# Kernel tuning notes

Hardware: AMD Instinct MI355X
Metric: run time of the kernel (lower is better)

## Reference

```python
import jax, jax.numpy as jnp
import numpy as np

N = 100000   # nodes
E = 1600000  # edges per view
B = 256      # graphs in batch
D = 128      # feature dim
H, C = 4, 32 # heads, per-head channels (H*C = 128)


def _seg_softmax(logits, seg, num_seg):
    # numerically stable softmax over segments (per-destination / per-graph)
    m = jax.ops.segment_max(logits, seg, num_segments=num_seg)
    e = jnp.exp(logits - m[seg])
    s = jax.ops.segment_sum(e, seg, num_segments=num_seg)
    return e / s[seg]


def _gat_conv(x, edge_index, W, att_src, att_dst, bias):
    # PyG GATConv with add_self_loops=True, concat heads
    n = x.shape[0]
    loop = jnp.arange(n, dtype=edge_index.dtype)
    src = jnp.concatenate([edge_index[0], loop])
    dst = jnp.concatenate([edge_index[1], loop])
    xh = (x @ W).reshape(n, H, C)                      # [N,H,C]
    a_src = jnp.einsum('nhc,hc->nh', xh, att_src)      # [N,H]
    a_dst = jnp.einsum('nhc,hc->nh', xh, att_dst)
    alpha = jax.nn.leaky_relu(a_src[src] + a_dst[dst], 0.2)   # [E+N,H]
    alpha = _seg_softmax(alpha, dst, n)
    msg = xh[src] * alpha[..., None]                   # [E+N,H,C]
    out = jax.ops.segment_sum(msg, dst, num_segments=n)
    return out.reshape(n, H * C) + bias


def _global_attention(h, batch, gate_W, gate_b):
    gate = (h @ gate_W + gate_b)[:, 0]                 # [N]
    a = _seg_softmax(gate, batch, B)
    return jax.ops.segment_sum(a[:, None] * h, batch, num_segments=B)  # [B,128]


def setup_inputs() -> dict:
    key = jax.random.key(0)
    ks = jax.random.split(key, 32)
    p = lambda k, shp: (jax.random.normal(k, shp, dtype=jnp.float32) * 0.05)
    inp = {
        'x': jax.random.normal(ks[0], (N, D), dtype=jnp.float32),
        'edge_index_ast': jax.random.randint(ks[1], (2, E), 0, N, dtype=jnp.int32),
        'edge_index_cfg': jax.random.randint(ks[2], (2, E), 0, N, dtype=jnp.int32),
        'edge_index_pdg': jax.random.randint(ks[3], (2, E), 0, N, dtype=jnp.int32),
        'batch': jnp.sort(jax.random.randint(ks[4], (N,), 0, B, dtype=jnp.int32)),
        'ln_g': jnp.ones((D,), jnp.float32),
        'ln_b': jnp.zeros((D,), jnp.float32),
        'proj_W': p(ks[5], (D, D)), 'proj_b': p(ks[6], (D,)),
        'W_ast': p(ks[7], (D, H * C)), 'att_src_ast': p(ks[8], (H, C)), 'att_dst_ast': p(ks[9], (H, C)), 'bias_ast': p(ks[10], (H * C,)),
        'W_cfg': p(ks[11], (D, H * C)), 'att_src_cfg': p(ks[12], (H, C)), 'att_dst_cfg': p(ks[13], (H, C)), 'bias_cfg': p(ks[14], (H * C,)),
        'W_pdg': p(ks[15], (D, H * C)), 'att_src_pdg': p(ks[16], (H, C)), 'att_dst_pdg': p(ks[17], (H, C)), 'bias_pdg': p(ks[18], (H * C,)),
        'gate_W': p(ks[19], (H * C, 1)), 'gate_b': p(ks[20], (1,)),
        'clf_W1': p(ks[21], (3 * H * C, 128)), 'clf_b1': p(ks[22], (128,)),
        'clf_W2': p(ks[23], (128, 1)), 'clf_b2': p(ks[24], (1,)),
    }
    return inp


def reference(x, edge_index_ast, edge_index_cfg, edge_index_pdg, batch,
              ln_g, ln_b, proj_W, proj_b,
              W_ast, att_src_ast, att_dst_ast, bias_ast,
              W_cfg, att_src_cfg, att_dst_cfg, bias_cfg,
              W_pdg, att_src_pdg, att_dst_pdg, bias_pdg,
              gate_W, gate_b, clf_W1, clf_b1, clf_W2, clf_b2):
    # LayerNorm + proj + LeakyReLU (dropout = eval/no-op)
    mu = jnp.mean(x, axis=-1, keepdims=True)
    var = jnp.var(x, axis=-1, keepdims=True)
    xn = (x - mu) * jax.lax.rsqrt(var + 1e-5) * ln_g + ln_b
    h0 = jax.nn.leaky_relu(xn @ proj_W + proj_b, 0.01)

    h_ast = jax.nn.elu(_gat_conv(h0, edge_index_ast, W_ast, att_src_ast, att_dst_ast, bias_ast))
    g_ast = _global_attention(h_ast, batch, gate_W, gate_b)
    h_cfg = jax.nn.elu(_gat_conv(h0, edge_index_cfg, W_cfg, att_src_cfg, att_dst_cfg, bias_cfg))
    g_cfg = _global_attention(h_cfg, batch, gate_W, gate_b)
    h_pdg = jax.nn.elu(_gat_conv(h0, edge_index_pdg, W_pdg, att_src_pdg, att_dst_pdg, bias_pdg))
    g_pdg = _global_attention(h_pdg, batch, gate_W, gate_b)

    combined = jnp.concatenate([g_ast, g_cfg, g_pdg], axis=1)  # [B, 384]
    hid = jax.nn.leaky_relu(combined @ clf_W1 + clf_b1, 0.01)
    return (hid @ clf_W2 + clf_b2).reshape(-1)                 # [B]
```

## Files before the change

kernel.cpp:

```cpp
#include <hip/hip_runtime.h>
#include <hip/hip_bf16.h>
#include <hip/hip_fp16.h>
#include <math.h>

#define NN 100000
#define EE 1600000
#define BB 256
#define NBUCK 391
#define PBLK 384
#define CH 4167
#define TOTB (3 * PBLK)
#define ROWS_PAD 100096
#define SCAP 4608
#define OBCAP (SCAP + 256)
#define LOG2E 1.442695041f
#define GEMM_BLKS 782
#define AGG_BLKS 25000
#define XH_ELEMS ((size_t)ROWS_PAD * 128)
#define A_ELEMS ((size_t)ROWS_PAD * 4)
#define HV_ELEMS ((size_t)NN * 128)

typedef short bf16x8 __attribute__((ext_vector_type(8)));
typedef float f32x4 __attribute__((ext_vector_type(4)));

__device__ __forceinline__ unsigned short f2bf(float f) {
    __hip_bfloat16 h = __float2bfloat16(f);
    return *(unsigned short*)&h;
}
__device__ __forceinline__ unsigned short f2h(float f) {
    __half h = __float2half(f);
    return *(unsigned short*)&h;
}
__device__ __forceinline__ float h2f(unsigned short u) {
    __half h = *(__half*)&u;
    return __half2float(h);
}

__global__ __launch_bounds__(256) void prep_kernel(const float* __restrict__ W0,
                                                   const float* __restrict__ W1,
                                                   const float* __restrict__ W2,
                                                   const float* __restrict__ W3,
                                                   const float* __restrict__ ln_g,
                                                   const float* __restrict__ ln_b,
                                                   unsigned short* __restrict__ WT,
                                                   float* __restrict__ c12) {
    if (blockIdx.x < 256) {
        int which = blockIdx.x >> 6;
        const float* W = which == 0 ? W0 : which == 1 ? W1 : which == 2 ? W2 : W3;
        int i = (blockIdx.x & 63) * 256 + threadIdx.x;
        int n = i >> 7, k = i & 127;
        float v = W[k * 128 + n];
        if (which == 0) v *= ln_g[k];
        WT[which * 16384 + i] = f2bf(v);
        return;
    }
    __shared__ float p1[256], p2[256];
    int t = threadIdx.x;
    int n = t & 127, kg = t >> 7;
    float c1 = 0.f, c2 = 0.f;
    for (int k = kg * 64; k < kg * 64 + 64; k++) {
        float w = W0[k * 128 + n];
        c1 = fmaf(ln_g[k], w, c1);
        c2 = fmaf(ln_b[k], w, c2);
    }
    p1[t] = c1; p2[t] = c2;
    __syncthreads();
    if (kg == 0) {
        c12[n] = p1[n] + p1[128 + n];
        c12[128 + n] = p2[n] + p2[128 + n];
    }
}


__device__ __forceinline__ void scatter_res_body(int bid, int tid,
                                                 const int* __restrict__ e0,
                                                 const int* __restrict__ e1,
                                                 const int* __restrict__ e2,
                                                 int* __restrict__ counters,
                                                 unsigned int* __restrict__ pairbuf) {
    int v = bid / PBLK, p = bid % PBLK;
    const int* ei = v == 0 ? e0 : v == 1 ? e1 : e2;
    __shared__ int hcnt[NBUCK];
    __shared__ int cur[NBUCK];
    for (int i = tid; i < NBUCK; i += 256) hcnt[i] = 0;
    __syncthreads();
    int ea = p * CH, ebnd = min(EE, ea + CH);
    int e = ea + tid;
    for (; e + 768 < ebnd; e += 1024) {
        int d0 = ei[EE + e], d1 = ei[EE + e + 256];
        int d2 = ei[EE + e + 512], d3 = ei[EE + e + 768];
        atomicAdd(&hcnt[((unsigned)d0) >> 8], 1);
        atomicAdd(&hcnt[((unsigned)d1) >> 8], 1);
        atomicAdd(&hcnt[((unsigned)d2) >> 8], 1);
        atomicAdd(&hcnt[((unsigned)d3) >> 8], 1);
    }
    for (; e < ebnd; e += 256) atomicAdd(&hcnt[((unsigned)ei[EE + e]) >> 8], 1);
    __syncthreads();
    int* gcnt = counters + v * NBUCK;
    for (int i = tid; i < NBUCK; i += 256) {
        int c = hcnt[i];
        cur[i] = c ? atomicAdd(&gcnt[i], c) : 0;
    }
    __syncthreads();
    unsigned int* pbuf = pairbuf + (size_t)v * NBUCK * SCAP;
    e = ea + tid;
    for (; e + 768 < ebnd; e += 1024) {
        unsigned s0 = (unsigned)ei[e],       d0 = (unsigned)ei[EE + e];
        unsigned s1 = (unsigned)ei[e + 256], d1 = (unsigned)ei[EE + e + 256];
        unsigned s2 = (unsigned)ei[e + 512], d2 = (unsigned)ei[EE + e + 512];
        unsigned s3 = (unsigned)ei[e + 768], d3 = (unsigned)ei[EE + e + 768];
        int p0 = atomicAdd(&cur[d0 >> 8], 1);
        int p1 = atomicAdd(&cur[d1 >> 8], 1);
        int p2 = atomicAdd(&cur[d2 >> 8], 1);
        int p3 = atomicAdd(&cur[d3 >> 8], 1);
        if (p0 < SCAP) pbuf[(size_t)(d0 >> 8) * SCAP + p0] = (s0 << 8) | (d0 & 255u);
        if (p1 < SCAP) pbuf[(size_t)(d1 >> 8) * SCAP + p1] = (s1 << 8) | (d1 & 255u);
        if (p2 < SCAP) pbuf[(size_t)(d2 >> 8) * SCAP + p2] = (s2 << 8) | (d2 & 255u);
        if (p3 < SCAP) pbuf[(size_t)(d3 >> 8) * SCAP + p3] = (s3 << 8) | (d3 & 255u);
    }
    for (; e < ebnd; e += 256) {
        unsigned s = (unsigned)ei[e], d = (unsigned)ei[EE + e];
        int pos = atomicAdd(&cur[d >> 8], 1);
        if (pos < SCAP) pbuf[(size_t)(d >> 8) * SCAP + pos] = (s << 8) | (d & 255u);
    }
}

__device__ __forceinline__ void proj_body(int nb, int tid,
                                          const float* __restrict__ X,
                                          const unsigned short* __restrict__ WT,
                                          const float* __restrict__ c12,
                                          const float* __restrict__ pb,
                                          unsigned short* __restrict__ Out) {
    int w = tid >> 6, lane = tid & 63;
    int ln = lane & 15, oct = lane >> 4;
    int row0 = nb * 128 + w * 32;

    f32x4 acc[2][8];
    #pragma unroll
    for (int i = 0; i < 2; i++)
        #pragma unroll
        for (int j = 0; j < 8; j++) acc[i][j] = (f32x4){0.f, 0.f, 0.f, 0.f};

    const float* X0 = X + (size_t)min(row0 + ln, NN - 1) * 128;
    const float* X1 = X + (size_t)min(row0 + 16 + ln, NN - 1) * 128;
    const bf16x8* Wr = (const bf16x8*)(WT + (size_t)ln * 128);

    float s0 = 0.f, q0 = 0.f, s1 = 0.f, q1 = 0.f;
    #pragma unroll
    for (int kq = 0; kq < 4; kq++) {
        int koff = kq * 4 + oct;
        float4 xa = *(const float4*)(X0 + koff * 8);
        float4 xb = *(const float4*)(X0 + koff * 8 + 4);
        float4 ya = *(const float4*)(X1 + koff * 8);
        float4 yb = *(const float4*)(X1 + koff * 8 + 4);
        s0 += (xa.x + xa.y) + (xa.z + xa.w) + (xb.x + xb.y) + (xb.z + xb.w);
        q0 += xa.x * xa.x + xa.y * xa.y + xa.z * xa.z + xa.w * xa.w
            + xb.x * xb.x + xb.y * xb.y + xb.z * xb.z + xb.w * xb.w;
        s1 += (ya.x + ya.y) + (ya.z + ya.w) + (yb.x + yb.y) + (yb.z + yb.w);
        q1 += ya.x * ya.x + ya.y * ya.y + ya.z * ya.z + ya.w * ya.w
            + yb.x * yb.x + yb.y * yb.y + yb.z * yb.z + yb.w * yb.w;
        bf16x8 a0, a1;
        a0[0] = (short)f2bf(xa.x); a0[1] = (short)f2bf(xa.y); a0[2] = (short)f2bf(xa.z); a0[3] = (short)f2bf(xa.w);
        a0[4] = (short)f2bf(xb.x); a0[5] = (short)f2bf(xb.y); a0[6] = (short)f2bf(xb.z); a0[7] = (short)f2bf(xb.w);
        a1[0] = (short)f2bf(ya.x); a1[1] = (short)f2bf(ya.y); a1[2] = (short)f2bf(ya.z); a1[3] = (short)f2bf(ya.w);
        a1[4] = (short)f2bf(yb.x); a1[5] = (short)f2bf(yb.y); a1[6] = (short)f2bf(yb.z); a1[7] = (short)f2bf(yb.w);
        #pragma unroll
        for (int ct = 0; ct < 8; ct++) {
            bf16x8 bfr = Wr[ct * 16 * 16 + koff];
            acc[0][ct] = __builtin_amdgcn_mfma_f32_16x16x32_bf16(a0, bfr, acc[0][ct], 0, 0, 0);
            acc[1][ct] = __builtin_amdgcn_mfma_f32_16x16x32_bf16(a1, bfr, acc[1][ct], 0, 0, 0);
        }
    }
    #pragma unroll
    for (int m = 16; m < 64; m <<= 1) {
        s0 += __shfl_xor(s0, m); q0 += __shfl_xor(q0, m);
        s1 += __shfl_xor(s1, m); q1 += __shfl_xor(q1, m);
    }
    float mu0 = s0 * (1.0f / 128.0f);
    float rs0 = rsqrtf(q0 * (1.0f / 128.0f) - mu0 * mu0 + 1e-5f);
    float mu1 = s1 * (1.0f / 128.0f);
    float rs1 = rsqrtf(q1 * (1.0f / 128.0f) - mu1 * mu1 + 1e-5f);

    float c1v[8], c2v[8], pbv[8];
    #pragma unroll
    for (int ct = 0; ct < 8; ct++) {
        c1v[ct] = c12[ct * 16 + ln];
        c2v[ct] = c12[128 + ct * 16 + ln];
        pbv[ct] = pb[ct * 16 + ln];
    }
    #pragma unroll
    for (int rt = 0; rt < 2; rt++) {
        #pragma unroll
        for (int r = 0; r < 4; r++) {
            int src = oct * 4 + r;
            float rs_r = __shfl(rt ? rs1 : rs0, src);
            float mu_r = __shfl(rt ? mu1 : mu0, src);
            int row = row0 + rt * 16 + oct * 4 + r;
            #pragma unroll
            for (int ct = 0; ct < 8; ct++) {
                float v = rs_r * acc[rt][ct][r] - rs_r * mu_r * c1v[ct] + c2v[ct] + pbv[ct];
                v = v > 0.f ? v : 0.01f * v;
                Out[(size_t)row * 128 + ct * 16 + ln] = f2bf(v);
            }
        }
    }
}

__device__ __forceinline__ void view_body(int nb, int tid,
                                          const unsigned short* __restrict__ h0,
                                          const unsigned short* __restrict__ WTv,
                                          const float* __restrict__ asw,
                                          const float* __restrict__ adw,
                                          unsigned short* __restrict__ Out,
                                          float* __restrict__ a_src,
                                          float* __restrict__ a_dst) {
    int w = tid >> 6, lane = tid & 63;
    int ln = lane & 15, oct = lane >> 4;
    int row0 = nb * 128 + w * 32;

    f32x4 acc[2][8];
    #pragma unroll
    for (int i = 0; i < 2; i++)
        #pragma unroll
        for (int j = 0; j < 8; j++) acc[i][j] = (f32x4){0.f, 0.f, 0.f, 0.f};

    const bf16x8* Ar0 = (const bf16x8*)(h0 + (size_t)(row0 + ln) * 128);
    const bf16x8* Ar1 = (const bf16x8*)(h0 + (size_t)(row0 + 16 + ln) * 128);
    const bf16x8* Wr  = (const bf16x8*)(WTv + (size_t)ln * 128);

    #pragma unroll
    for (int kq = 0; kq < 4; kq++) {
        int koff = kq * 4 + oct;
        bf16x8 a0 = Ar0[koff];
        bf16x8 a1 = Ar1[koff];
        #pragma unroll
        for (int ct = 0; ct < 8; ct++) {
            bf16x8 bfr = Wr[ct * 16 * 16 + koff];
            acc[0][ct] = __builtin_amdgcn_mfma_f32_16x16x32_bf16(a0, bfr, acc[0][ct], 0, 0, 0);
            acc[1][ct] = __builtin_amdgcn_mfma_f32_16x16x32_bf16(a1, bfr, acc[1][ct], 0, 0, 0);
        }
    }
    float aswv[8], adwv[8];
    #pragma unroll
    for (int ct = 0; ct < 8; ct++) {
        aswv[ct] = asw[ct * 16 + ln] * LOG2E;
        adwv[ct] = adw[ct * 16 + ln] * LOG2E;
    }

    #pragma unroll
    for (int rt = 0; rt < 2; rt++) {
        #pragma unroll
        for (int r = 0; r < 4; r++) {
            int row = row0 + rt * 16 + oct * 4 + r;
            float sh_[4] = {0.f, 0.f, 0.f, 0.f}, dh_[4] = {0.f, 0.f, 0.f, 0.f};
            #pragma unroll
            for (int ct = 0; ct < 8; ct++) {
                float vv = acc[rt][ct][r];
                Out[(size_t)row * 128 + ct * 16 + ln] = f2h(vv);
                sh_[ct >> 1] = fmaf(vv, aswv[ct], sh_[ct >> 1]);
                dh_[ct >> 1] = fmaf(vv, adwv[ct], dh_[ct >> 1]);
            }
            #pragma unroll
            for (int off = 1; off < 16; off <<= 1) {
                #pragma unroll
                for (int h = 0; h < 4; h++) {
                    sh_[h] += __shfl_xor(sh_[h], off);
                    dh_[h] += __shfl_xor(dh_[h], off);
                }
            }
            if (ln == 0) {
                *(float4*)(a_src + (size_t)row * 4) = make_float4(sh_[0], sh_[1], sh_[2], sh_[3]);
                *(float4*)(a_dst + (size_t)row * 4) = make_float4(dh_[0], dh_[1], dh_[2], dh_[3]);
            }
        }
    }
}

__device__ __forceinline__ void fine_body(int bid, int t,
                                          const unsigned int* __restrict__ pairbuf,
                                          const int* __restrict__ counters,
                                          int* __restrict__ deg3,
                                          int* __restrict__ start3,
                                          unsigned int* __restrict__ ebuf3) {
    int v = bid / NBUCK, b = bid - v * NBUCK;
    int cnt = min(counters[v * NBUCK + b], SCAP);
    const unsigned int* pb = pairbuf + (size_t)(v * NBUCK + b) * SCAP;
    unsigned int* eb = ebuf3 + (size_t)(v * NBUCK + b) * OBCAP;
    int obase = (v * NBUCK + b) * OBCAP;
    __shared__ int hist[256], cur[256];
    __shared__ int wsum[4];
    int node = b * 256 + t;
    int valid = (node < NN) ? 1 : 0;
    hist[t] = valid;
    __syncthreads();
    {
        int i = t;
        for (; i + 768 < cnt; i += 1024) {
            unsigned v0 = pb[i], v1 = pb[i + 256], v2 = pb[i + 512], v3 = pb[i + 768];
            atomicAdd(&hist[v0 & 255u], 1);
            atomicAdd(&hist[v1 & 255u], 1);
            atomicAdd(&hist[v2 & 255u], 1);
            atomicAdd(&hist[v3 & 255u], 1);
        }
        for (; i < cnt; i += 256) atomicAdd(&hist[pb[i] & 255u], 1);
    }
    __syncthreads();
    int hv = hist[t];
    int lanev = t & 63, wv = t >> 6;
    int incl = hv;
    #pragma unroll
    for (int m = 1; m < 64; m <<= 1) {
        int u = __shfl_up(incl, m);
        if (lanev >= m) incl += u;
    }
    if (lanev == 63) wsum[wv] = incl;
    __syncthreads();
    int prefix = 0;
    #pragma unroll
    for (int i = 0; i < 4; i++) prefix += (i < wv) ? wsum[i] : 0;
    int excl = incl + prefix - hv;
    cur[t] = excl + valid;
    if (valid) eb[excl] = (((unsigned)node) << 8) | ((unsigned)node & 255u);
    __syncthreads();
    {
        int i = t;
        for (; i + 768 < cnt; i += 1024) {
            unsigned v0 = pb[i], v1 = pb[i + 256], v2 = pb[i + 512], v3 = pb[i + 768];
            int p0 = atomicAdd(&cur[v0 & 255u], 1);
            int p1 = atomicAdd(&cur[v1 & 255u], 1);
            int p2 = atomicAdd(&cur[v2 & 255u], 1);
            int p3 = atomicAdd(&cur[v3 & 255u], 1);
            eb[p0] = v0; eb[p1] = v1; eb[p2] = v2; eb[p3] = v3;
        }
        for (; i < cnt; i += 256) {
            unsigned int val = pb[i];
            int pos = atomicAdd(&cur[val & 255u], 1);
            eb[pos] = val;
        }
    }
    if (valid) {
        deg3[v * NN + node] = hv;
        start3[v * NN + node] = obase + excl;
    }
}

__device__ __forceinline__ void agg_body(int node, int tid,
                                         const unsigned short* __restrict__ xh,
                                         const int* __restrict__ start,
                                         const int* __restrict__ deg,
                                         const unsigned int* __restrict__ ebuf,
                                         const float* __restrict__ a_src,
                                         const float* __restrict__ a_dst,
                                         const float* __restrict__ bias,
                                         const float* __restrict__ gw,
                                         const float* __restrict__ gb,
                                         unsigned short* __restrict__ hvb,
                                         float* __restrict__ gexpv,
                                         float* wlds) {
    int lane = tid & 63;
    int h = lane >> 4;
    int st = start[node];
    int cnt = deg[node];
    const char* xb = (const char*)xh;
    int laneoff = lane * 4;
    float4 ad4 = *(const float4*)(a_dst + (size_t)node * 4);
    float* ww = wlds + (tid >> 6) * 272;
    const float* wr = ww + h * 68;

    float accx = 0.f, accy = 0.f, den = 0.f;
    for (int j0 = 0; j0 < cnt; j0 += 64) {
        int nj = min(64, cnt - j0);
        int src_l = 0;
        if (lane < nj) {
            src_l = (int)(ebuf[st + j0 + lane] >> 8);
            float4 as4 = *(const float4*)(a_src + (size_t)src_l * 4);
            float t0 = as4.x + ad4.x, t1 = as4.y + ad4.y;
            float t2 = as4.z + ad4.z, t3 = as4.w + ad4.w;
            t0 = fmaxf(t0, 0.f) + 0.2f * fminf(t0, 0.f);
            t1 = fmaxf(t1, 0.f) + 0.2f * fminf(t1, 0.f);
            t2 = fmaxf(t2, 0.f) + 0.2f * fminf(t2, 0.f);
            t3 = fmaxf(t3, 0.f) + 0.2f * fminf(t3, 0.f);
            ww[0 * 68 + lane] = exp2f(t0);
            ww[1 * 68 + lane] = exp2f(t1);
            ww[2 * 68 + lane] = exp2f(t2);
            ww[3 * 68 + lane] = exp2f(t3);
        }
        int jj = 0;
        for (; jj + 8 <= nj; jj += 8) {
            int s0 = __builtin_amdgcn_readlane(src_l, jj);
            int s1 = __builtin_amdgcn_readlane(src_l, jj + 1);
            int s2 = __builtin_amdgcn_readlane(src_l, jj + 2);
            int s3 = __builtin_amdgcn_readlane(src_l, jj + 3);
            int s4 = __builtin_amdgcn_readlane(src_l, jj + 4);
            int s5 = __builtin_amdgcn_readlane(src_l, jj + 5);
            int s6 = __builtin_amdgcn_readlane(src_l, jj + 6);
            int s7 = __builtin_amdgcn_readlane(src_l, jj + 7);
            __half2 x0 = *(const __half2*)(xb + (((size_t)(unsigned)s0) << 8) + laneoff);
            __half2 x1 = *(const __half2*)(xb + (((size_t)(unsigned)s1) << 8) + laneoff);
            __half2 x2 = *(const __half2*)(xb + (((size_t)(unsigned)s2) << 8) + laneoff);
            __half2 x3 = *(const __half2*)(xb + (((size_t)(unsigned)s3) << 8) + laneoff);
            __half2 x4 = *(const __half2*)(xb + (((size_t)(unsigned)s4) << 8) + laneoff);
            __half2 x5 = *(const __half2*)(xb + (((size_t)(unsigned)s5) << 8) + laneoff);
            __half2 x6 = *(const __half2*)(xb + (((size_t)(unsigned)s6) << 8) + laneoff);
            __half2 x7 = *(const __half2*)(xb + (((size_t)(unsigned)s7) << 8) + laneoff);
            float4 wa = *(const float4*)(wr + jj);
            float4 wb = *(const float4*)(wr + jj + 4);
            den += (wa.x + wa.y) + (wa.z + wa.w) + (wb.x + wb.y) + (wb.z + wb.w);
            accx = fmaf(__low2float(x0), wa.x, accx);
            accy = fmaf(__high2float(x0), wa.x, accy);
            accx = fmaf(__low2float(x1), wa.y, accx);
            accy = fmaf(__high2float(x1), wa.y, accy);
            accx = fmaf(__low2float(x2), wa.z, accx);
            accy = fmaf(__high2float(x2), wa.z, accy);
            accx = fmaf(__low2float(x3), wa.w, accx);
            accy = fmaf(__high2float(x3), wa.w, accy);
            accx = fmaf(__low2float(x4), wb.x, accx);
            accy = fmaf(__high2float(x4), wb.x, accy);
            accx = fmaf(__low2float(x5), wb.y, accx);
            accy = fmaf(__high2float(x5), wb.y, accy);
            accx = fmaf(__low2float(x6), wb.z, accx);
            accy = fmaf(__high2float(x6), wb.z, accy);
            accx = fmaf(__low2float(x7), wb.w, accx);
            accy = fmaf(__high2float(x7), wb.w, accy);
        }
        for (; jj + 4 <= nj; jj += 4) {
            int s0 = __builtin_amdgcn_readlane(src_l, jj);
            int s1 = __builtin_amdgcn_readlane(src_l, jj + 1);
            int s2 = __builtin_amdgcn_readlane(src_l, jj + 2);
            int s3 = __builtin_amdgcn_readlane(src_l, jj + 3);
            __half2 x0 = *(const __half2*)(xb + (((size_t)(unsigned)s0) << 8) + laneoff);
            __half2 x1 = *(const __half2*)(xb + (((size_t)(unsigned)s1) << 8) + laneoff);
            __half2 x2 = *(const __half2*)(xb + (((size_t)(unsigned)s2) << 8) + laneoff);
            __half2 x3 = *(const __half2*)(xb + (((size_t)(unsigned)s3) << 8) + laneoff);
            float4 wa = *(const float4*)(wr + jj);
            den += (wa.x + wa.y) + (wa.z + wa.w);
            accx = fmaf(__low2float(x0), wa.x, accx);
            accy = fmaf(__high2float(x0), wa.x, accy);
            accx = fmaf(__low2float(x1), wa.y, accx);
            accy = fmaf(__high2float(x1), wa.y, accy);
            accx = fmaf(__low2float(x2), wa.z, accx);
            accy = fmaf(__high2float(x2), wa.z, accy);
            accx = fmaf(__low2float(x3), wa.w, accx);
            accy = fmaf(__high2float(x3), wa.w, accy);
        }
        for (; jj < nj; jj++) {
            int s = __builtin_amdgcn_readlane(src_l, jj);
            float w = wr[jj];
            __half2 xv = *(const __half2*)(xb + (((size_t)(unsigned)s) << 8) + laneoff);
            den += w;
            accx = fmaf(__low2float(xv), w, accx);
            accy = fmaf(__high2float(xv), w, accy);
        }
    }
    float inv = 1.0f / den;
    float2 bb = *(const float2*)(bias + lane * 2);
    float o0 = accx * inv + bb.x;
    float o1 = accy * inv + bb.y;
    o0 = o0 > 0.f ? o0 : exp2f(o0 * LOG2E) - 1.0f;
    o1 = o1 > 0.f ? o1 : exp2f(o1 * LOG2E) - 1.0f;
    unsigned int packed = (unsigned)f2h(o0) | ((unsigned)f2h(o1) << 16);
    *(unsigned int*)(hvb + (size_t)node * 128 + lane * 2) = packed;
    float2 g2 = *(const float2*)(gw + lane * 2);
    float gp = o0 * g2.x + o1 * g2.y;
    #pragma unroll
    for (int m = 1; m < 64; m <<= 1) gp += __shfl_xor(gp, m);
    if (lane == 0) gexpv[node] = exp2f((gp + gb[0]) * LOG2E);
}

__device__ __forceinline__ void pool_body(int b, int tid,
                                          const unsigned short* __restrict__ hvb,
                                          const float* __restrict__ gexpv,
                                          const int* __restrict__ batch,
                                          float* __restrict__ gout,
                                          int voff,
                                          float* sacc, float* sws) {
    int g = tid >> 7;
    int ch = tid & 127;
    int l = 0, r = NN;
    while (l < r) { int m = (l + r) >> 1; if (batch[m] < b) l = m + 1; else r = m; }
    int s0 = l;
    r = NN;
    while (l < r) { int m = (l + r) >> 1; if (batch[m] < b + 1) l = m + 1; else r = m; }
    int s1 = l;
    float acc = 0.f, wsum = 0.f;
    for (int n = s0 + g; n < s1; n += 8) {
        float w = gexpv[n];
        wsum += w;
        acc = fmaf(w, h2f(hvb[(size_t)n * 128 + ch]), acc);
    }
    sacc[g * 128 + ch] = acc;
    if (ch == 0) sws[g] = wsum;
    __syncthreads();
    if (g == 0) {
        float a = 0.f, w = 0.f;
        #pragma unroll
        for (int i = 0; i < 8; i++) { a += sacc[i * 128 + ch]; w += sws[i]; }
        gout[b * 384 + voff + ch] = (s1 > s0) ? a / w : 0.f;
    }
}

__global__ __launch_bounds__(256) void fat_scatter_proj(const int* e0, const int* e1, const int* e2,
                                                        int* counters, unsigned int* pairbuf,
                                                        const float* X, const unsigned short* WT,
                                                        const float* c12, const float* pb,
                                                        unsigned short* h0) {
    if (blockIdx.x < TOTB) scatter_res_body(blockIdx.x, threadIdx.x, e0, e1, e2, counters, pairbuf);
    else proj_body(blockIdx.x - TOTB, threadIdx.x, X, WT, c12, pb, h0);
}

__global__ __launch_bounds__(256) void fat_fine_view3(const unsigned int* pairbuf, const int* counters,
                                                      int* deg3, int* start3, unsigned int* ebuf3,
                                                      const unsigned short* h0, const unsigned short* WT,
                                                      const float* as0, const float* ad0,
                                                      const float* as1, const float* ad1,
                                                      const float* as2, const float* ad2,
                                                      unsigned short* xh3, float* a_src3, float* a_dst3) {
    if (blockIdx.x < 3 * NBUCK) {
        fine_body(blockIdx.x, threadIdx.x, pairbuf, counters, deg3, start3, ebuf3);
        return;
    }
    int t = blockIdx.x - 3 * NBUCK;
    int v = t / GEMM_BLKS;
    int nb = t - v * GEMM_BLKS;
    const float* as_ = v == 0 ? as0 : v == 1 ? as1 : as2;
    const float* ad_ = v == 0 ? ad0 : v == 1 ? ad1 : ad2;
    view_body(nb, threadIdx.x, h0, WT + (size_t)(1 + v) * 16384, as_, ad_,
              xh3 + (size_t)v * XH_ELEMS,
              a_src3 + (size_t)v * A_ELEMS, a_dst3 + (size_t)v * A_ELEMS);
}

__global__ __launch_bounds__(256) void aggregate3_kernel(const unsigned short* __restrict__ xh3,
                                                         const int* __restrict__ start3,
                                                         const int* __restrict__ deg3,
                                                         const unsigned int* __restrict__ ebuf3,
                                                         const float* __restrict__ a_src3,
                                                         const float* __restrict__ a_dst3,
                                                         const float* __restrict__ b0,
                                                         const float* __restrict__ b1,
                                                         const float* __restrict__ b2,
                                                         const float* __restrict__ gw,
                                                         const float* __restrict__ gb,
                                                         unsigned short* __restrict__ hvb3,
                                                         float* __restrict__ gexpv3) {
    __shared__ float wlds[4 * 272];
    int v = blockIdx.x / AGG_BLKS;
    int bin = blockIdx.x - v * AGG_BLKS;
    int node = (bin * 256 + threadIdx.x) >> 6;
    if (node >= NN) return;
    const float* bias = v == 0 ? b0 : v == 1 ? b1 : b2;
    agg_body(node, threadIdx.x,
             xh3 + (size_t)v * XH_ELEMS,
             start3 + v * NN, deg3 + v * NN,
             ebuf3,
             a_src3 + (size_t)v * A_ELEMS, a_dst3 + (size_t)v * A_ELEMS,
             bias, gw, gb,
             hvb3 + (size_t)v * HV_ELEMS, gexpv3 + v * NN, wlds);
}

__global__ __launch_bounds__(1024) void pool3_kernel(const unsigned short* __restrict__ hvb3,
                                                     const float* __restrict__ gexpv3,
                                                     const int* __restrict__ batch,
                                                     float* __restrict__ gout) {
    __shared__ float sacc[8 * 128];
    __shared__ float sws[8];
    int v = blockIdx.x >> 8;
    int b = blockIdx.x & 255;
    pool_body(b, threadIdx.x, hvb3 + (size_t)v * HV_ELEMS, gexpv3 + v * NN,
              batch, gout, v * 128, sacc, sws);
}

__global__ __launch_bounds__(128) void clf_kernel(const float* __restrict__ gout,
                                                  const float* __restrict__ W1,
                                                  const float* __restrict__ b1,
                                                  const float* __restrict__ W2,
                                                  const float* __restrict__ b2,
                                                  float* __restrict__ out) {
    int b = blockIdx.x;
    int j = threadIdx.x;
    float acc = b1[j];
    for (int k = 0; k < 384; k++) acc = fmaf(gout[b * 384 + k], W1[k * 128 + j], acc);
    acc = acc > 0.f ? acc : 0.01f * acc;
    float p = acc * W2[j];
    #pragma unroll
    for (int m = 1; m < 64; m <<= 1) p += __shfl_xor(p, m);
    __shared__ float sh[2];
    if ((j & 63) == 0) sh[j >> 6] = p;
    __syncthreads();
    if (j == 0) out[b] = sh[0] + sh[1] + b2[0];
}

extern "C" void kernel_launch(void* const* d_in, const int* in_sizes, int n_in,
                              void* d_out, int out_size, void* d_ws, size_t ws_size,
                              hipStream_t stream) {
    const float* x      = (const float*)d_in[0];
    const int*   ei[3]  = {(const int*)d_in[1], (const int*)d_in[2], (const int*)d_in[3]};
    const int*   batch  = (const int*)d_in[4];
    const float* ln_g   = (const float*)d_in[5];
    const float* ln_b   = (const float*)d_in[6];
    const float* proj_W = (const float*)d_in[7];
    const float* proj_b = (const float*)d_in[8];
    const float* Wv[3]  = {(const float*)d_in[9],  (const float*)d_in[13], (const float*)d_in[17]};
    const float* asv[3] = {(const float*)d_in[10], (const float*)d_in[14], (const float*)d_in[18]};
    const float* adv[3] = {(const float*)d_in[11], (const float*)d_in[15], (const float*)d_in[19]};
    const float* bv[3]  = {(const float*)d_in[12], (const float*)d_in[16], (const float*)d_in[20]};
    const float* gate_W = (const float*)d_in[21];
    const float* gate_b = (const float*)d_in[22];
    const float* clf_W1 = (const float*)d_in[23];
    const float* clf_b1 = (const float*)d_in[24];
    const float* clf_W2 = (const float*)d_in[25];
    const float* clf_b2 = (const float*)d_in[26];
    float* out = (float*)d_out;

    (void)in_sizes; (void)n_in; (void)out_size; (void)ws_size;

    char* base = (char*)d_ws;
    size_t off = 0;
    auto nxt = [&](size_t bytes) { char* r = base + off; off += (bytes + 255) & ~(size_t)255; return r; };

    unsigned short* h0   = (unsigned short*)nxt((size_t)ROWS_PAD * 128 * 2);
    unsigned short* xh3  = (unsigned short*)nxt((size_t)3 * XH_ELEMS * 2);
    unsigned short* hvb3 = (unsigned short*)nxt((size_t)3 * HV_ELEMS * 2);
    unsigned short* WT   = (unsigned short*)nxt(4 * 16384 * 2);
    float* c12    = (float*)nxt(256 * 4);
    float* a_src3 = (float*)nxt((size_t)3 * A_ELEMS * 4);
    float* a_dst3 = (float*)nxt((size_t)3 * A_ELEMS * 4);
    float* gexpv3 = (float*)nxt((size_t)3 * NN * 4);
    float* gout   = (float*)nxt(BB * 384 * 4);
    int* counters = (int*)nxt(3 * NBUCK * 4);
    int* deg3     = (int*)nxt(3 * NN * 4);
    int* start3   = (int*)nxt(3 * NN * 4);
    unsigned int* ebuf3   = (unsigned int*)nxt((size_t)3 * NBUCK * OBCAP * 4);
    unsigned int* pairbuf = (unsigned int*)nxt((size_t)3 * NBUCK * SCAP * 4);

    hipMemsetAsync(counters, 0, 3 * NBUCK * 4, stream);
    prep_kernel<<<257, 256, 0, stream>>>(proj_W, Wv[0], Wv[1], Wv[2], ln_g, ln_b, WT, c12);
    fat_scatter_proj<<<TOTB + GEMM_BLKS, 256, 0, stream>>>(ei[0], ei[1], ei[2], counters, pairbuf,
                                                           x, WT, c12, proj_b, h0);
    fat_fine_view3<<<3 * NBUCK + 3 * GEMM_BLKS, 256, 0, stream>>>(
        pairbuf, counters, deg3, start3, ebuf3, h0, WT,
        asv[0], adv[0], asv[1], adv[1], asv[2], adv[2],
        xh3, a_src3, a_dst3);
    aggregate3_kernel<<<3 * AGG_BLKS, 256, 0, stream>>>(xh3, start3, deg3, ebuf3,
                                                        a_src3, a_dst3,
                                                        bv[0], bv[1], bv[2],
                                                        gate_W, gate_b, hvb3, gexpv3);
    pool3_kernel<<<3 * 256, 1024, 0, stream>>>(hvb3, gexpv3, batch, gout);
    clf_kernel<<<256, 128, 0, stream>>>(gout, clf_W1, clf_b1, clf_W2, clf_b2, out);
}
```

Baseline: 609.8 us.

## Fuse attention pooling into aggregation via atomic accumulation per graph

Removes the separate pooling kernel and the fp16 node-feature buffer. Each aggregated node now atomically adds its gated features and gate weight into per-graph accumulators, and the classifier normalizes them. This avoids writing and rereading the full hidden features, at the cost of heavy float atomic contention on a small set of addresses and nondeterministic summation order.

```diff
diff --git a/kernel.cpp b/kernel.cpp
--- a/kernel.cpp
+++ b/kernel.cpp
@@ -18,7 +18,6 @@
 #define AGG_BLKS 25000
 #define XH_ELEMS ((size_t)ROWS_PAD * 128)
 #define A_ELEMS ((size_t)ROWS_PAD * 4)
-#define HV_ELEMS ((size_t)NN * 128)
 
 typedef short bf16x8 __attribute__((ext_vector_type(8)));
 typedef float f32x4 __attribute__((ext_vector_type(4)));
@@ -30,10 +29,6 @@
 __device__ __forceinline__ unsigned short f2h(float f) {
     __half h = __float2half(f);
     return *(unsigned short*)&h;
-}
-__device__ __forceinline__ float h2f(unsigned short u) {
-    __half h = *(__half*)&u;
-    return __half2float(h);
 }
 
 __global__ __launch_bounds__(256) void prep_kernel(const float* __restrict__ W0,
@@ -344,7 +339,7 @@
     }
 }
 
-__device__ __forceinline__ void agg_body(int node, int tid,
+__device__ __forceinline__ void agg_body(int node, int tid, int v,
                                          const unsigned short* __restrict__ xh,
                                          const int* __restrict__ start,
                                          const int* __restrict__ deg,
@@ -354,8 +349,9 @@
                                          const float* __restrict__ bias,
                                          const float* __restrict__ gw,
                                          const float* __restrict__ gb,
-                                         unsigned short* __restrict__ hvb,
-                                         float* __restrict__ gexpv,
+                                         const int* __restrict__ batch,
+                                         float* __restrict__ gacc,
+                                         float* __restrict__ gws,
                                          float* wlds) {
     int lane = tid & 63;
     int h = lane >> 4;
@@ -458,45 +454,16 @@
     float o1 = accy * inv + bb.y;
     o0 = o0 > 0.f ? o0 : exp2f(o0 * LOG2E) - 1.0f;
     o1 = o1 > 0.f ? o1 : exp2f(o1 * LOG2E) - 1.0f;
-    unsigned int packed = (unsigned)f2h(o0) | ((unsigned)f2h(o1) << 16);
-    *(unsigned int*)(hvb + (size_t)node * 128 + lane * 2) = packed;
     float2 g2 = *(const float2*)(gw + lane * 2);
     float gp = o0 * g2.x + o1 * g2.y;
     #pragma unroll
     for (int m = 1; m < 64; m <<= 1) gp += __shfl_xor(gp, m);
-    if (lane == 0) gexpv[node] = exp2f((gp + gb[0]) * LOG2E);
-}
-
-__device__ __forceinline__ void pool_body(int b, int tid,
-                                          const unsigned short* __restrict__ hvb,
-                                          const float* __restrict__ gexpv,
-                                          const int* __restrict__ batch,
-                                          float* __restrict__ gout,
-                                          int voff,
-                                          float* sacc, float* sws) {
-    int g = tid >> 7;
-    int ch = tid & 127;
-    int l = 0, r = NN;
-    while (l < r) { int m = (l + r) >> 1; if (batch[m] < b) l = m + 1; else r = m; }
-    int s0 = l;
-    r = NN;
-    while (l < r) { int m = (l + r) >> 1; if (batch[m] < b + 1) l = m + 1; else r = m; }
-    int s1 = l;
-    float acc = 0.f, wsum = 0.f;
-    for (int n = s0 + g; n < s1; n += 8) {
-        float w = gexpv[n];
-        wsum += w;
-        acc = fmaf(w, h2f(hvb[(size_t)n * 128 + ch]), acc);
-    }
-    sacc[g * 128 + ch] = acc;
-    if (ch == 0) sws[g] = wsum;
-    __syncthreads();
-    if (g == 0) {
-        float a = 0.f, w = 0.f;
-        #pragma unroll
-        for (int i = 0; i < 8; i++) { a += sacc[i * 128 + ch]; w += sws[i]; }
-        gout[b * 384 + voff + ch] = (s1 > s0) ? a / w : 0.f;
-    }
+    float gexp = exp2f((gp + gb[0]) * LOG2E);
+    int b = batch[node];
+    float* gr = gacc + (size_t)b * 384 + v * 128;
+    atomicAdd(&gr[lane * 2],     o0 * gexp);
+    atomicAdd(&gr[lane * 2 + 1], o1 * gexp);
+    if (lane == 0) atomicAdd(&gws[b * 3 + v], gexp);
 }
 
 __global__ __launch_bounds__(256) void fat_scatter_proj(const int* e0, const int* e1, const int* e2,
@@ -540,36 +507,25 @@
                                                          const float* __restrict__ b2,
                                                          const float* __restrict__ gw,
                                                          const float* __restrict__ gb,
-                                                         unsigned short* __restrict__ hvb3,
-                                                         float* __restrict__ gexpv3) {
+                                                         const int* __restrict__ batch,
+                                                         float* __restrict__ gacc,
+                                                         float* __restrict__ gws) {
     __shared__ float wlds[4 * 272];
     int v = blockIdx.x / AGG_BLKS;
     int bin = blockIdx.x - v * AGG_BLKS;
     int node = (bin * 256 + threadIdx.x) >> 6;
     if (node >= NN) return;
     const float* bias = v == 0 ? b0 : v == 1 ? b1 : b2;
-    agg_body(node, threadIdx.x,
+    agg_body(node, threadIdx.x, v,
              xh3 + (size_t)v * XH_ELEMS,
              start3 + v * NN, deg3 + v * NN,
              ebuf3,
              a_src3 + (size_t)v * A_ELEMS, a_dst3 + (size_t)v * A_ELEMS,
-             bias, gw, gb,
-             hvb3 + (size_t)v * HV_ELEMS, gexpv3 + v * NN, wlds);
-}
-
-__global__ __launch_bounds__(1024) void pool3_kernel(const unsigned short* __restrict__ hvb3,
-                                                     const float* __restrict__ gexpv3,
-                                                     const int* __restrict__ batch,
-                                                     float* __restrict__ gout) {
-    __shared__ float sacc[8 * 128];
-    __shared__ float sws[8];
-    int v = blockIdx.x >> 8;
-    int b = blockIdx.x & 255;
-    pool_body(b, threadIdx.x, hvb3 + (size_t)v * HV_ELEMS, gexpv3 + v * NN,
-              batch, gout, v * 128, sacc, sws);
-}
-
-__global__ __launch_bounds__(128) void clf_kernel(const float* __restrict__ gout,
+             bias, gw, gb, batch, gacc, gws, wlds);
+}
+
+__global__ __launch_bounds__(128) void clf_kernel(const float* __restrict__ gacc,
+                                                  const float* __restrict__ gws,
                                                   const float* __restrict__ W1,
                                                   const float* __restrict__ b1,
                                                   const float* __restrict__ W2,
@@ -577,8 +533,14 @@
                                                   float* __restrict__ out) {
     int b = blockIdx.x;
     int j = threadIdx.x;
+    float w0 = gws[b * 3 + 0], w1 = gws[b * 3 + 1], w2 = gws[b * 3 + 2];
+    float i0 = w0 > 0.f ? 1.0f / w0 : 0.f;
+    float i1 = w1 > 0.f ? 1.0f / w1 : 0.f;
+    float i2 = w2 > 0.f ? 1.0f / w2 : 0.f;
     float acc = b1[j];
-    for (int k = 0; k < 384; k++) acc = fmaf(gout[b * 384 + k], W1[k * 128 + j], acc);
+    for (int k = 0; k < 128; k++)       acc = fmaf(gacc[b * 384 + k] * i0, W1[k * 128 + j], acc);
+    for (int k = 128; k < 256; k++)     acc = fmaf(gacc[b * 384 + k] * i1, W1[k * 128 + j], acc);
+    for (int k = 256; k < 384; k++)     acc = fmaf(gacc[b * 384 + k] * i2, W1[k * 128 + j], acc);
     acc = acc > 0.f ? acc : 0.01f * acc;
     float p = acc * W2[j];
     #pragma unroll
@@ -619,20 +581,20 @@
 
     unsigned short* h0   = (unsigned short*)nxt((size_t)ROWS_PAD * 128 * 2);
     unsigned short* xh3  = (unsigned short*)nxt((size_t)3 * XH_ELEMS * 2);
-    unsigned short* hvb3 = (unsigned short*)nxt((size_t)3 * HV_ELEMS * 2);
     unsigned short* WT   = (unsigned short*)nxt(4 * 16384 * 2);
     float* c12    = (float*)nxt(256 * 4);
     float* a_src3 = (float*)nxt((size_t)3 * A_ELEMS * 4);
     float* a_dst3 = (float*)nxt((size_t)3 * A_ELEMS * 4);
-    float* gexpv3 = (float*)nxt((size_t)3 * NN * 4);
-    float* gout   = (float*)nxt(BB * 384 * 4);
-    int* counters = (int*)nxt(3 * NBUCK * 4);
+    char*  zbase  = (char*)nxt((3 * NBUCK + BB * 384 + BB * 3) * 4);
+    int*   counters = (int*)zbase;
+    float* gacc     = (float*)(zbase + 3 * NBUCK * 4);
+    float* gws      = (float*)(zbase + (3 * NBUCK + BB * 384) * 4);
     int* deg3     = (int*)nxt(3 * NN * 4);
     int* start3   = (int*)nxt(3 * NN * 4);
     unsigned int* ebuf3   = (unsigned int*)nxt((size_t)3 * NBUCK * OBCAP * 4);
     unsigned int* pairbuf = (unsigned int*)nxt((size_t)3 * NBUCK * SCAP * 4);
 
-    hipMemsetAsync(counters, 0, 3 * NBUCK * 4, stream);
+    hipMemsetAsync(zbase, 0, (3 * NBUCK + BB * 384 + BB * 3) * 4, stream);
     prep_kernel<<<257, 256, 0, stream>>>(proj_W, Wv[0], Wv[1], Wv[2], ln_g, ln_b, WT, c12);
     fat_scatter_proj<<<TOTB + GEMM_BLKS, 256, 0, stream>>>(ei[0], ei[1], ei[2], counters, pairbuf,
                                                            x, WT, c12, proj_b, h0);
@@ -643,7 +605,6 @@
     aggregate3_kernel<<<3 * AGG_BLKS, 256, 0, stream>>>(xh3, start3, deg3, ebuf3,
                                                         a_src3, a_dst3,
                                                         bv[0], bv[1], bv[2],
-                                                        gate_W, gate_b, hvb3, gexpv3);
-    pool3_kernel<<<3 * 256, 1024, 0, stream>>>(hvb3, gexpv3, batch, gout);
-    clf_kernel<<<256, 128, 0, stream>>>(gout, clf_W1, clf_b1, clf_W2, clf_b2, out);
-}
+                                                        gate_W, gate_b, batch, gacc, gws);
+    clf_kernel<<<256, 128, 0, stream>>>(gacc, gws, clf_W1, clf_b1, clf_W2, clf_b2, out);
+}
```

New measurement: 1.086 ms. +78.1%, slower.
